# Performance work log

Measured on AMD Instinct MI355X. Metric: run time of the kernel, lower is better.

## Reference

```python
import jax, jax.numpy as jnp
import numpy as np

KNN = 11  # self.knn in VoronoiBaseNN


def setup_inputs() -> dict:
    key = jax.random.key(0)
    k1, k2 = jax.random.split(key)
    points = jax.random.normal(k1, (2, 50000, 3), dtype=jnp.float32)   # GT surface samples
    spoints = jax.random.normal(k2, (2, 4000, 3), dtype=jnp.float32)   # Voronoi generators
    return {"points": points, "spoints": spoints}


def reference(points, spoints):
    # Pairwise squared distances: [B, N, M]
    d2 = ((points[:, :, None, :] - spoints[:, None, :, :]) ** 2).sum(-1)
    # KNN smallest, sorted ascending (torch.topk(largest=False, sorted=True))
    _, idx = jax.lax.top_k(-d2, KNN)            # idx: [B, N, KNN]
    # Gather the KNN generator coordinates: [B, N, KNN, 3]
    gathered = jax.vmap(lambda sp, i: sp[i])(spoints, idx)
    inside = gathered[:, :, 0, :]               # closest cell center [B, N, 3]
    point_to_center = points - inside           # [B, N, 3]
    # Voronoi edge vectors to the other KNN-1 neighbors: [B, N, KNN-1, 3]
    voronoi_edge = gathered[:, :, 1:, :] - inside[:, :, None, :]
    edge_l = jnp.sqrt((voronoi_edge ** 2).sum(-1))                      # [B, N, KNN-1]
    vector_length = (point_to_center[:, :, None, :] * voronoi_edge).sum(-1) / edge_l
    sq_dist = (vector_length - edge_l / 2.0) ** 2
    return sq_dist.min(-1)                      # [B, N]
```

## Files before the change

### kernel.cpp

```cpp
#include <hip/hip_runtime.h>
#include <math.h>

#define NPTS  50000
#define NSP   4000
#define NGRP  1000
#define NW    8
#define QW    (NGRP / NW)
#define KNN   11
#define BIG   3.4e38f
#define SEGCAP 96
#define SEGPAD 8
#define SEGSTR (SEGCAP + SEGPAD)
#define GRIDC 32
#define NKEY  65536
#define NGB   ((NPTS + 63) / 64)

#define MED3(a,b,c) __builtin_amdgcn_fmed3f((a),(b),(c))

__device__ unsigned g_hist[NKEY];
__device__ float4   g_sorted[2 * NPTS];

static __device__ __forceinline__ unsigned spread5(unsigned v) {
    return (v & 1u) | ((v & 2u) << 2) | ((v & 4u) << 4) |
           ((v & 8u) << 6) | ((v & 16u) << 8);
}
static __device__ __forceinline__ unsigned morton15(float x, float y, float z) {
    int gx = (int)floorf((x + 4.0f) * 4.0f);
    int gy = (int)floorf((y + 4.0f) * 4.0f);
    int gz = (int)floorf((z + 4.0f) * 4.0f);
    gx = min(max(gx, 0), GRIDC - 1);
    gy = min(max(gy, 0), GRIDC - 1);
    gz = min(max(gz, 0), GRIDC - 1);
    return spread5((unsigned)gx) | (spread5((unsigned)gy) << 1) |
           (spread5((unsigned)gz) << 2);
}

__global__ __launch_bounds__(1024, 1) void k_sort(const float* __restrict__ pts) {
    __shared__ unsigned h[32768];
    __shared__ unsigned ps[1024];
    const int b = blockIdx.x;
    const int t = threadIdx.x;
    const float* __restrict__ pb = pts + (size_t)b * NPTS * 3;

#pragma unroll
    for (int i = 0; i < 32; ++i) h[t + i * 1024] = 0u;
    __syncthreads();

    for (int n = t; n < NPTS; n += 1024) {
        const float x = pb[n * 3], y = pb[n * 3 + 1], z = pb[n * 3 + 2];
        atomicAdd(&h[morton15(x, y, z)], 1u);
    }
    __syncthreads();

    unsigned s = 0;
#pragma unroll
    for (int j = 0; j < 32; ++j) s += h[t * 32 + j];
    ps[t] = s;
    __syncthreads();
    for (int off = 1; off < 1024; off <<= 1) {
        const unsigned v = (t >= off) ? ps[t - off] : 0u;
        __syncthreads();
        ps[t] += v;
        __syncthreads();
    }
    unsigned run = ps[t] - s;
#pragma unroll
    for (int j = 0; j < 32; ++j) {
        const unsigned c = h[t * 32 + j];
        h[t * 32 + j] = run;
        run += c;
    }
    __syncthreads();

    for (int n = t; n < NPTS; n += 1024) {
        const float x = pb[n * 3], y = pb[n * 3 + 1], z = pb[n * 3 + 2];
        const unsigned dst = atomicAdd(&h[morton15(x, y, z)], 1u);
        g_sorted[(size_t)b * NPTS + dst] =
            make_float4(x, y, z, __uint_as_float((unsigned)n));
    }
}

__global__ void k_zero() {
    int t = blockIdx.x * 256 + threadIdx.x;
    if (t < NKEY) g_hist[t] = 0u;
}
__global__ void k_hist(const float* __restrict__ pts) {
    int n = blockIdx.x * 256 + threadIdx.x;
    if (n >= 2 * NPTS) return;
    const float* p = pts + (size_t)n * 3;
    int b = (n >= NPTS) ? 1 : 0;
    atomicAdd(&g_hist[((unsigned)b << 15) | morton15(p[0], p[1], p[2])], 1u);
}
__global__ void k_scan() {
    __shared__ unsigned part[1024];
    const int t = threadIdx.x;
    const unsigned base = (unsigned)blockIdx.x * 32768u + (unsigned)t * 32u;
    unsigned s = 0;
#pragma unroll
    for (int j = 0; j < 32; ++j) s += g_hist[base + j];
    part[t] = s;
    __syncthreads();
    for (int off = 1; off < 1024; off <<= 1) {
        unsigned v = (t >= off) ? part[t - off] : 0u;
        __syncthreads();
        part[t] += v;
        __syncthreads();
    }
    unsigned run = (unsigned)blockIdx.x * (unsigned)NPTS + part[t] - s;
#pragma unroll
    for (int j = 0; j < 32; ++j) {
        unsigned h = g_hist[base + j];
        g_hist[base + j] = run;
        run += h;
    }
}
__global__ void k_scatter(const float* __restrict__ pts) {
    int n = blockIdx.x * 256 + threadIdx.x;
    if (n >= 2 * NPTS) return;
    const float* p = pts + (size_t)n * 3;
    int b = (n >= NPTS) ? 1 : 0;
    float x = p[0], y = p[1], z = p[2];
    unsigned dst = atomicAdd(&g_hist[((unsigned)b << 15) | morton15(x, y, z)], 1u);
    if (dst < 2u * NPTS)
        g_sorted[dst] = make_float4(x, y, z, __uint_as_float((unsigned)(n - b * NPTS)));
}

static __device__ __forceinline__ float wred_min(float v) {
#pragma unroll
    for (int off = 32; off > 0; off >>= 1) v = fminf(v, __shfl_xor(v, off, 64));
    return v;
}
static __device__ __forceinline__ float wred_max(float v) {
#pragma unroll
    for (int off = 32; off > 0; off >>= 1) v = fmaxf(v, __shfl_xor(v, off, 64));
    return v;
}

__global__ __launch_bounds__(512, 6) void voronoi_kernel(
    const float* __restrict__ spts,
    float* __restrict__ out)
{
    __shared__ float4 sl[NW * SEGSTR];
    __shared__ float  lds_d[NW][64][11];
    __shared__ int    lds_i[NW][64];
    __shared__ float  lds_m[NW];

    float (*lds_b)[64] = (float (*)[64])lds_i;

    const int b    = blockIdx.y;
    const int lane = threadIdx.x & 63;
    const int wq   = threadIdx.x >> 6;
    const int grp  = (int)(((unsigned)blockIdx.x * 401u) % (unsigned)NGB);
    int pi = grp * 64 + lane;
    const bool valid = (pi < NPTS);
    if (!valid) pi = NPTS - 1;

    const float4 P = g_sorted[(size_t)b * NPTS + pi];
    const float px = P.x, py = P.y, pz = P.z;
    const unsigned orig = __float_as_uint(P.w);

    const float mnx = wred_min(px), mxx = wred_max(px);
    const float mny = wred_min(py), mxy = wred_max(py);
    const float mnz = wred_min(pz), mxz = wred_max(pz);
    const float ccx = 0.5f * (mnx + mxx);
    const float ccy = 0.5f * (mny + mxy);
    const float ccz = 0.5f * (mnz + mxz);
    const float R = sqrtf(wred_max(
        fmaf(px - ccx, px - ccx, fmaf(py - ccy, py - ccy, (pz - ccz) * (pz - ccz)))));

    const float4* __restrict__ spq = (const float4*)(spts + (size_t)b * NSP * 3);
    const int g0 = wq * QW, g1 = g0 + QW;

    float myMin = BIG;
    for (int k0 = g0; k0 < g1; k0 += 64) {
        const int g  = k0 + lane;
        const int gc = (g < g1) ? g : (g1 - 1);
        const float4 q0 = spq[3 * gc + 0];
        const float4 q1 = spq[3 * gc + 1];
        const float4 q2 = spq[3 * gc + 2];
        float dx = q0.x - ccx, dy = q0.y - ccy, dz = q0.z - ccz;
        float md = fmaf(dx, dx, fmaf(dy, dy, dz * dz));
        dx = q0.w - ccx; dy = q1.x - ccy; dz = q1.y - ccz;
        md = fminf(md, fmaf(dx, dx, fmaf(dy, dy, dz * dz)));
        dx = q1.z - ccx; dy = q1.w - ccy; dz = q2.x - ccz;
        md = fminf(md, fmaf(dx, dx, fmaf(dy, dy, dz * dz)));
        dx = q2.y - ccx; dy = q2.z - ccy; dz = q2.w - ccz;
        md = fminf(md, fmaf(dx, dx, fmaf(dy, dy, dz * dz)));
        if (g < g1) myMin = fminf(myMin, md);
    }
    float vv = myMin, m11 = 0.0f;
#pragma unroll
    for (int t = 0; t < KNN; ++t) {
        m11 = wred_min(vv);
        vv = (vv == m11) ? BIG : vv;
    }
    if (lane == 0) lds_m[wq] = m11;
    __syncthreads();
    float m11g = BIG;
#pragma unroll
    for (int q = 0; q < NW; ++q) m11g = fminf(m11g, lds_m[q]);
    const float Trad = sqrtf(m11g) + R;
    const float T = Trad * Trad * 1.0004f + 1e-12f;

#define ADM(sx, sy, sz) \
    (fmaf(MED3((sx), mnx, mxx) - (sx), MED3((sx), mnx, mxx) - (sx), \
     fmaf(MED3((sy), mny, mxy) - (sy), MED3((sy), mny, mxy) - (sy), \
          (MED3((sz), mnz, mxz) - (sz)) * (MED3((sz), mnz, mxz) - (sz)))) <= T)

    const int segbase = wq * SEGSTR;
    unsigned cnt = 0;

    auto padseg = [&]() {
        if (lane < SEGPAD)
            sl[segbase + (int)cnt + lane] =
                make_float4(1e18f, 1e18f, 1e18f, __uint_as_float(0x7fffffffu));
    };

#define PUSH(sx, sy, sz, ok, idx, CONSUME) { \
        const unsigned long long msk = __ballot(ok); \
        const unsigned np = (unsigned)__popcll(msk); \
        if (cnt + np > (unsigned)SEGCAP) {               \
            padseg(); CONSUME(cnt); cnt = 0; of = true; \
        } \
        if (ok) { \
            const unsigned pos = cnt + \
                __builtin_amdgcn_mbcnt_hi((unsigned)(msk >> 32), \
                    __builtin_amdgcn_mbcnt_lo((unsigned)msk, 0u)); \
            sl[segbase + (int)pos] = \
                make_float4((sx), (sy), (sz), __uint_as_float((unsigned)(idx))); \
        } \
        cnt += np; }

#define RUN_BUILD(CONSUME, ofvar) { \
        ofvar = false; bool& of = ofvar; cnt = 0; \
        for (int k0 = g0; k0 < g1; k0 += 64) { \
            const int g  = k0 + lane; \
            const int gc = (g < g1) ? g : (g1 - 1); \
            const bool in = (g < g1); \
            const float4 q0 = spq[3 * gc + 0]; \
            const float4 q1 = spq[3 * gc + 1]; \
            const float4 q2 = spq[3 * gc + 2]; \
            const bool a0 = in && ADM(q0.x, q0.y, q0.z); \
            const bool a1 = in && ADM(q0.w, q1.x, q1.y); \
            const bool a2 = in && ADM(q1.z, q1.w, q2.x); \
            const bool a3 = in && ADM(q2.y, q2.z, q2.w); \
            PUSH(q0.x, q0.y, q0.z, a0, 4 * gc + 0, CONSUME); \
            PUSH(q0.w, q1.x, q1.y, a1, 4 * gc + 1, CONSUME); \
            PUSH(q1.z, q1.w, q2.x, a2, 4 * gc + 2, CONSUME); \
            PUSH(q2.y, q2.z, q2.w, a3, 4 * gc + 3, CONSUME); \
        } \
        padseg(); CONSUME(cnt); }

    float d0 = BIG, d1 = BIG, d2 = BIG, d3 = BIG, d4 = BIG, d5 = BIG,
          d6 = BIG, d7 = BIG, d8 = BIG, d9 = BIG, d10 = BIG;
    int i0 = 0x7fffffff;

#define CHAIN(nd, jj) { \
        if (__ballot((nd) < d10)) { \
            d10 = MED3(d9, d10, (nd)); \
            d9  = MED3(d8, d9,  (nd)); \
            d8  = MED3(d7, d8,  (nd)); \
            d7  = MED3(d6, d7,  (nd)); \
            d6  = MED3(d5, d6,  (nd)); \
            d5  = MED3(d4, d5,  (nd)); \
            d4  = MED3(d3, d4,  (nd)); \
            d3  = MED3(d2, d3,  (nd)); \
            d2  = MED3(d1, d2,  (nd)); \
            d1  = MED3(d0, d1,  (nd)); \
            i0  = ((nd) < d0) ? (jj) : i0; \
            d0  = fminf(d0, (nd)); \
        } }
#define CANDA(c) { \
        const float dx = px - (c).x, dy = py - (c).y, dz = pz - (c).z; \
        const float nd = fmaf(dx, dx, fmaf(dy, dy, dz * dz)); \
        const int jj = (int)__float_as_uint((c).w); \
        CHAIN(nd, jj); }

    auto chainA = [&](unsigned n) {
        if (n == 0u) return;
        float4 e0 = sl[segbase + 0], e1 = sl[segbase + 1],
               e2 = sl[segbase + 2], e3 = sl[segbase + 3];
        for (unsigned k = 0; k < n; k += 4) {
            const float4 n0 = sl[segbase + (int)k + 4];
            const float4 n1 = sl[segbase + (int)k + 5];
            const float4 n2 = sl[segbase + (int)k + 6];
            const float4 n3 = sl[segbase + (int)k + 7];
            CANDA(e0); CANDA(e1); CANDA(e2); CANDA(e3);
            e0 = n0; e1 = n1; e2 = n2; e3 = n3;
        }
    };

    bool ovfA;
    RUN_BUILD(chainA, ovfA);
    const unsigned cntA = cnt;

    lds_d[wq][lane][0]  = d0;  lds_d[wq][lane][1]  = d1;
    lds_d[wq][lane][2]  = d2;  lds_d[wq][lane][3]  = d3;
    lds_d[wq][lane][4]  = d4;  lds_d[wq][lane][5]  = d5;
    lds_d[wq][lane][6]  = d6;  lds_d[wq][lane][7]  = d7;
    lds_d[wq][lane][8]  = d8;  lds_d[wq][lane][9]  = d9;
    lds_d[wq][lane][10] = d10;
    lds_i[wq][lane] = i0;
    __syncthreads();

    float gb = BIG; int gi = 0x7fffffff;
#pragma unroll
    for (int q = 0; q < NW; ++q) {
        const float dq = lds_d[q][lane][0];
        const int   iq = lds_i[q][lane];
        const bool take = (dq < gb) || (dq == gb && iq < gi);
        gb = take ? dq : gb;
        gi = take ? iq : gi;
    }
#define INS(v) { \
        d10 = MED3(d9, d10, (v)); \
        d9  = MED3(d8, d9,  (v)); \
        d8  = MED3(d7, d8,  (v)); \
        d7  = MED3(d6, d7,  (v)); \
        d6  = MED3(d5, d6,  (v)); \
        d5  = MED3(d4, d5,  (v)); \
        d4  = MED3(d3, d4,  (v)); \
        d3  = MED3(d2, d3,  (v)); \
        d2  = MED3(d1, d2,  (v)); \
        d1  = MED3(d0, d1,  (v)); \
        d0  = fminf(d0, (v)); }
#pragma unroll
    for (int q = 0; q < NW; ++q) {
        if (q == wq) continue;
#pragma unroll
        for (int k = 0; k < 11; ++k) {
            const float v = lds_d[q][lane][k];
            if (!__ballot(v < d10)) break;
            INS(v);
        }
    }
    const float d10g = d10;
    const int   i0g  = gi;

    const float* ip = spts + (size_t)b * NSP * 3 + (size_t)(unsigned)i0g * 3;
    const float ix = ip[0], iy = ip[1], iz = ip[2];
    const float vx = px - ix, vy = py - iy, vz = pz - iz;
    float best = BIG;

#define CANDB(c) { \
        const float dx = px - (c).x, dy = py - (c).y, dz = pz - (c).z; \
        const float nd = fmaf(dx, dx, fmaf(dy, dy, dz * dz)); \
        const int jj = (int)__float_as_uint((c).w); \
        const bool adm = (nd <= d10g) && (jj != i0g); \
        if (__ballot(adm)) { \
            const float ex = (c).x - ix, ey = (c).y - iy, ez = (c).z - iz; \
            const float ee = fmaf(ex, ex, fmaf(ey, ey, ez * ez)); \
            const float dt = fmaf(vx, ex, fmaf(vy, ey, vz * ez)); \
            const float u  = fmaf(-0.5f, ee, dt); \
            const float t2 = u * u * __builtin_amdgcn_rcpf(ee); \
            best = adm ? fminf(best, t2) : best; \
        } }

    auto scanB = [&](unsigned n) {
        if (n == 0u) return;
        float4 e0 = sl[segbase + 0], e1 = sl[segbase + 1],
               e2 = sl[segbase + 2], e3 = sl[segbase + 3];
        for (unsigned k = 0; k < n; k += 4) {
            const float4 n0 = sl[segbase + (int)k + 4];
            const float4 n1 = sl[segbase + (int)k + 5];
            const float4 n2 = sl[segbase + (int)k + 6];
            const float4 n3 = sl[segbase + (int)k + 7];
            CANDB(e0); CANDB(e1); CANDB(e2); CANDB(e3);
            e0 = n0; e1 = n1; e2 = n2; e3 = n3;
        }
    };

    if (!ovfA) {
        scanB(cntA);
    } else {
        bool ovfB;
        RUN_BUILD(scanB, ovfB);
        (void)ovfB;
    }

    __syncthreads();
    lds_b[wq][lane] = best;
    __syncthreads();
    if (wq == 0) {
        float m = lds_b[0][lane];
#pragma unroll
        for (int q = 1; q < NW; ++q) m = fminf(m, lds_b[q][lane]);
        if (valid) out[(size_t)b * NPTS + orig] = m;
    }
}

extern "C" void kernel_launch(void* const* d_in, const int* in_sizes, int n_in,
                              void* d_out, int out_size, void* d_ws, size_t ws_size,
                              hipStream_t stream) {
    (void)in_sizes; (void)n_in; (void)d_ws; (void)ws_size; (void)out_size;
    const float* pts  = (const float*)d_in[0];
    const float* spts = (const float*)d_in[1];
    float* out = (float*)d_out;

    (void)hipGetLastError();
    k_sort<<<dim3(2), dim3(1024), 0, stream>>>(pts);
    if (hipGetLastError() != hipSuccess) {
        k_zero   <<<dim3(NKEY / 256),            dim3(256),  0, stream>>>();
        k_hist   <<<dim3((2 * NPTS + 255)/256),  dim3(256),  0, stream>>>(pts);
        k_scan   <<<dim3(2),                     dim3(1024), 0, stream>>>();
        k_scatter<<<dim3((2 * NPTS + 255)/256),  dim3(256),  0, stream>>>(pts);
    }
    voronoi_kernel<<<dim3(NGB, 2), dim3(512), 0, stream>>>(spts, out);
}
```

Before: 285.1 us.

## Parallelize Morton sort across 16 blocks with cooperative grid sync

Replaces the two-block shared-memory counting sort with a cooperative kernel of 16 blocks that build a global histogram with atomics, scan it in two blocks, and scatter points. Grid-wide syncs separate the phases. The aim is to spread the histogram and scatter passes over more CUs instead of serialising them on two. In exchange it uses global atomics and pays for grid barriers, with the multi-kernel path kept as a fallback if the cooperative launch fails.

```diff
diff --git a/kernel.cpp b/kernel.cpp
--- a/kernel.cpp
+++ b/kernel.cpp
@@ -1,4 +1,5 @@
 #include <hip/hip_runtime.h>
+#include <hip/hip_cooperative_groups.h>
 #include <math.h>
 
 #define NPTS  50000
@@ -14,6 +15,7 @@
 #define GRIDC 32
 #define NKEY  65536
 #define NGB   ((NPTS + 63) / 64)
+#define SORTB 16
 
 #define MED3(a,b,c) __builtin_amdgcn_fmed3f((a),(b),(c))
 
@@ -35,48 +37,56 @@
            (spread5((unsigned)gz) << 2);
 }
 
-__global__ __launch_bounds__(1024, 1) void k_sort(const float* __restrict__ pts) {
-    __shared__ unsigned h[32768];
-    __shared__ unsigned ps[1024];
-    const int b = blockIdx.x;
-    const int t = threadIdx.x;
+__global__ __launch_bounds__(1024, 1) void k_sortm(const float* __restrict__ pts) {
+    cooperative_groups::grid_group gg = cooperative_groups::this_grid();
+    __shared__ unsigned part[1024];
+    const int blk = blockIdx.x;
+    const int b   = blk >> 3;
+    const int sub = blk & 7;
+    const int t   = threadIdx.x;
+
+#pragma unroll
+    for (int i = 0; i < 4; ++i) g_hist[blk * 4096 + i * 1024 + t] = 0u;
+    gg.sync();
+
     const float* __restrict__ pb = pts + (size_t)b * NPTS * 3;
-
-#pragma unroll
-    for (int i = 0; i < 32; ++i) h[t + i * 1024] = 0u;
-    __syncthreads();
-
-    for (int n = t; n < NPTS; n += 1024) {
+    const int n0 = sub * (NPTS / 8);
+    const int n1 = (sub == 7) ? NPTS : n0 + (NPTS / 8);
+    for (int n = n0 + t; n < n1; n += 1024) {
         const float x = pb[n * 3], y = pb[n * 3 + 1], z = pb[n * 3 + 2];
-        atomicAdd(&h[morton15(x, y, z)], 1u);
-    }
-    __syncthreads();
-
-    unsigned s = 0;
-#pragma unroll
-    for (int j = 0; j < 32; ++j) s += h[t * 32 + j];
-    ps[t] = s;
-    __syncthreads();
-    for (int off = 1; off < 1024; off <<= 1) {
-        const unsigned v = (t >= off) ? ps[t - off] : 0u;
+        atomicAdd(&g_hist[((unsigned)b << 15) | morton15(x, y, z)], 1u);
+    }
+    gg.sync();
+
+    if (blk < 2) {
+        const unsigned base = (unsigned)blk * 32768u + (unsigned)t * 32u;
+        unsigned s = 0;
+#pragma unroll
+        for (int j = 0; j < 32; ++j) s += g_hist[base + j];
+        part[t] = s;
         __syncthreads();
-        ps[t] += v;
-        __syncthreads();
-    }
-    unsigned run = ps[t] - s;
-#pragma unroll
-    for (int j = 0; j < 32; ++j) {
-        const unsigned c = h[t * 32 + j];
-        h[t * 32 + j] = run;
-        run += c;
-    }
-    __syncthreads();
-
-    for (int n = t; n < NPTS; n += 1024) {
+        for (int off = 1; off < 1024; off <<= 1) {
+            const unsigned v = (t >= off) ? part[t - off] : 0u;
+            __syncthreads();
+            part[t] += v;
+            __syncthreads();
+        }
+        unsigned run = (unsigned)blk * (unsigned)NPTS + part[t] - s;
+#pragma unroll
+        for (int j = 0; j < 32; ++j) {
+            const unsigned h = g_hist[base + j];
+            g_hist[base + j] = run;
+            run += h;
+        }
+    }
+    gg.sync();
+
+    for (int n = n0 + t; n < n1; n += 1024) {
         const float x = pb[n * 3], y = pb[n * 3 + 1], z = pb[n * 3 + 2];
-        const unsigned dst = atomicAdd(&h[morton15(x, y, z)], 1u);
-        g_sorted[(size_t)b * NPTS + dst] =
-            make_float4(x, y, z, __uint_as_float((unsigned)n));
+        const unsigned dst =
+            atomicAdd(&g_hist[((unsigned)b << 15) | morton15(x, y, z)], 1u);
+        if (dst < 2u * NPTS)
+            g_sorted[dst] = make_float4(x, y, z, __uint_as_float((unsigned)n));
     }
 }
 
@@ -397,9 +407,12 @@
     const float* spts = (const float*)d_in[1];
     float* out = (float*)d_out;
 
-    (void)hipGetLastError();
-    k_sort<<<dim3(2), dim3(1024), 0, stream>>>(pts);
-    if (hipGetLastError() != hipSuccess) {
+    const float* pts_arg = pts;
+    void* args[] = { (void*)&pts_arg };
+    hipError_t ce = hipLaunchCooperativeKernel((const void*)k_sortm,
+                                               dim3(SORTB), dim3(1024), args,
+                                               0, stream);
+    if (ce != hipSuccess) {
         k_zero   <<<dim3(NKEY / 256),            dim3(256),  0, stream>>>();
         k_hist   <<<dim3((2 * NPTS + 255)/256),  dim3(256),  0, stream>>>(pts);
         k_scan   <<<dim3(2),                     dim3(1024), 0, stream>>>();
```

Result: no change. 289.6 us (+1.6%).
